# Optimization experiments

Measured on AMD Instinct MI355X. Metric: run time of the kernel, lower is better.

Reference implementation:

```python
import jax, jax.numpy as jnp
import numpy as np

B, T, N, M = 128, 128, 32, 128  # batch, window(input_len), driving_series, hidden_size


def _lstm_cell(x_t, h, c, Wih, Whh, bih, bhh):
    # PyTorch gate order: i, f, g, o
    g = x_t @ Wih.T + bih + h @ Whh.T + bhh
    i, f, gg, o = jnp.split(g, 4, axis=-1)
    c = jax.nn.sigmoid(f) * c + jax.nn.sigmoid(i) * jnp.tanh(gg)
    h = jax.nn.sigmoid(o) * jnp.tanh(c)
    return h, c


def _lstm_seq(x, Wih, Whh, bih, bhh):
    # x: [B,T,n] -> outputs [B,T,m], zero init state
    Bc = x.shape[0]
    m = Whh.shape[1]
    def step(carry, x_t):
        h, c = carry
        h, c = _lstm_cell(x_t, h, c, Wih, Whh, bih, bhh)
        return (h, c), h
    h0 = jnp.zeros((Bc, m), x.dtype)
    (_, _), ys = jax.lax.scan(step, (h0, h0), jnp.swapaxes(x, 0, 1))
    return jnp.swapaxes(ys, 0, 1)


def _forward(x, Wih0, Whh0, bih0, bhh0, We, Ue, Ve,
             Wg, bg, Wa, ba,
             Wih1, Whh1, bih1, bhh1, Wih2, Whh2, bih2, bhh2):
    Bc, Tc, n = x.shape
    m = Whh0.shape[1]
    ux = jnp.einsum('btn,mn->btm', x, Ue)  # Ue(x), constant across steps

    def step(carry, x_t):
        h, c = carry
        hs = jnp.concatenate([h, c], axis=-1)              # [B,2m]
        e = jnp.tanh(ux + (hs @ We.T)[:, None, :]) @ Ve[0]  # [B,T]
        a = jax.nn.softmax(e, axis=1)
        ia_t = jnp.einsum('bt,btn->bn', a, x)              # attended input at step t
        h, c = _lstm_cell(x_t, h, c, Wih0, Whh0, bih0, bhh0)
        return (h, c), ia_t

    h0 = jnp.zeros((Bc, m), x.dtype)
    (_, _), ia = jax.lax.scan(step, (h0, h0), jnp.swapaxes(x, 0, 1))
    input_attention = jnp.swapaxes(ia, 0, 1)               # [B,T,n]

    # self (spatial) attention, fully vectorized over t
    g = jnp.tanh(jnp.einsum('btn,mn->btm', x, Wg) + bg)
    a = jax.nn.sigmoid(jnp.einsum('btm,nm->btn', g, Wa) + ba)
    self_attention = a * x                                  # [B,T,n]

    out1 = _lstm_seq(input_attention, Wih1, Whh1, bih1, bhh1)
    out2 = _lstm_seq(self_attention, Wih2, Whh2, bih2, bhh2)
    return jnp.concatenate([out1, out2], axis=-1)           # [B,T,2m]


def setup_inputs() -> dict:
    key = jax.random.key(0)
    ks = jax.random.split(key, 20)
    stdv = 1.0 / np.sqrt(M)
    u = lambda k, shp: jax.random.uniform(k, shp, jnp.float32, -stdv, stdv)
    inp = {
        'x': jax.random.normal(ks[0], (B, T, N), jnp.float32),
        'Wih0': u(ks[1], (4 * M, N)), 'Whh0': u(ks[2], (4 * M, M)),
        'bih0': u(ks[3], (4 * M,)), 'bhh0': u(ks[4], (4 * M,)),
        'We': u(ks[5], (M, 2 * M)), 'Ue': u(ks[6], (M, N)), 'Ve': u(ks[7], (1, M)),
        'Wg': u(ks[8], (M, N)), 'bg': u(ks[9], (M,)),
        'Wa': u(ks[10], (N, M)), 'ba': u(ks[11], (N,)),
        'Wih1': u(ks[12], (4 * M, N)), 'Whh1': u(ks[13], (4 * M, M)),
        'bih1': u(ks[14], (4 * M,)), 'bhh1': u(ks[15], (4 * M,)),
        'Wih2': u(ks[16], (4 * M, N)), 'Whh2': u(ks[17], (4 * M, M)),
        'bih2': u(ks[18], (4 * M,)), 'bhh2': u(ks[19], (4 * M,)),
    }
    return inp


def reference(x, Wih0, Whh0, bih0, bhh0, We, Ue, Ve, Wg, bg, Wa, ba,
              Wih1, Whh1, bih1, bhh1, Wih2, Whh2, bih2, bhh2):
    return _forward(x, Wih0, Whh0, bih0, bhh0, We, Ue, Ve, Wg, bg, Wa, ba,
                    Wih1, Whh1, bih1, bhh1, Wih2, Whh2, bih2, bhh2)
```

## Files before the change

kernel.cpp:

```cpp
#include <hip/hip_runtime.h>

#define DI __device__ __forceinline__

DI float fsig(float v)  { return 1.0f / (1.0f + __expf(-v)); }
DI float ftanh(float v) { return 1.0f - 2.0f / (__expf(2.0f * v) + 1.0f); }

template <int MODE>
DI void lstm_scan(const float* __restrict__ xin,
                  const float* __restrict__ Wih,
                  const float* __restrict__ Whh,
                  const float* __restrict__ bih,
                  const float* __restrict__ bhh,
                  float* __restrict__ rec,
                  float* __restrict__ outp,
                  float* lds)
{
    const int tid = threadIdx.x;
    float* xl  = lds;
    float* h   = lds + 4096;
    float* c   = lds + 4224;
    float* act = lds + 4352;

    for (int i = tid; i < 4096; i += 512) xl[i] = xin[i];
    if (tid < 128) { h[tid] = 0.f; c[tid] = 0.f; }

    float4 wi[8], wh[32];
    {
        const float4* p = (const float4*)(Wih + tid * 32);
        #pragma unroll
        for (int i = 0; i < 8; ++i) wi[i] = p[i];
        const float4* q2 = (const float4*)(Whh + tid * 128);
        #pragma unroll
        for (int i = 0; i < 32; ++i) wh[i] = q2[i];
    }
    const float bias = bih[tid] + bhh[tid];
    const int gate = tid >> 7;
    __syncthreads();

    for (int t = 0; t < 128; ++t) {
        if (MODE == 0) {
            if (tid < 256) rec[t * 256 + tid] = (tid < 128) ? h[tid] : c[tid - 128];
        }
        float acc = bias;
        const float4* x4 = (const float4*)(xl + t * 32);
        #pragma unroll
        for (int i = 0; i < 8; ++i) {
            float4 v = x4[i];
            acc += wi[i].x * v.x + wi[i].y * v.y + wi[i].z * v.z + wi[i].w * v.w;
        }
        const float4* h4 = (const float4*)h;
        #pragma unroll
        for (int i = 0; i < 32; ++i) {
            float4 v = h4[i];
            acc += wh[i].x * v.x + wh[i].y * v.y + wh[i].z * v.z + wh[i].w * v.w;
        }
        float a = (gate == 2) ? ftanh(acc) : fsig(acc);
        act[tid] = a;
        __syncthreads();
        if (tid < 128) {
            float iv = act[tid], fv = act[128 + tid], gv = act[256 + tid], ov = act[384 + tid];
            float cn = fv * c[tid] + iv * gv;
            float hn = ov * ftanh(cn);
            c[tid] = cn; h[tid] = hn;
            if (MODE == 1) outp[t * 256 + tid] = hn;
        }
        __syncthreads();
    }
}

DI void selfatt_body(const float* __restrict__ x, const float* __restrict__ Wg,
                     const float* __restrict__ bg, const float* __restrict__ Wa,
                     const float* __restrict__ ba, float* __restrict__ sa,
                     int b, float* s)
{
    float* xl  = s;
    float* Wgl = s + 4224;
    float* WaT = s + 8448;
    float* bgl = s + 12672;
    float* bal = s + 12800;
    float* gl  = s + 12832;
    float* pp  = s + 13344;

    const int tid = threadIdx.x;
    for (int i = tid; i < 4096; i += 512) {
        int r = i >> 5, n = i & 31;
        xl[r * 33 + n]  = x[b * 4096 + i];
        Wgl[r * 33 + n] = Wg[i];
        WaT[(i & 127) * 33 + (i >> 7)] = Wa[i];
    }
    if (tid < 128) bgl[tid] = bg[tid];
    else if (tid < 160) bal[tid - 128] = ba[tid - 128];
    __syncthreads();

    const int tl = tid >> 7;
    for (int it = 0; it < 32; ++it) {
        {   const int m = tid & 127;
            const int t = it * 4 + tl;
            float acc = bgl[m];
            #pragma unroll
            for (int n = 0; n < 32; ++n) acc += xl[t * 33 + n] * Wgl[m * 33 + n];
            gl[tl * 128 + m] = ftanh(acc);
        }
        __syncthreads();
        {   const int n = tid & 31, c = (tid >> 5) & 3;
            float acc = 0.f;
            #pragma unroll
            for (int j = 0; j < 32; ++j) {
                int m = c * 32 + j;
                acc += gl[tl * 128 + m] * WaT[m * 33 + n];
            }
            pp[(tl * 4 + c) * 32 + n] = acc;
        }
        __syncthreads();
        if (tid < 128) {
            const int tl2 = tid >> 5, n = tid & 31;
            const int t = it * 4 + tl2;
            float sv = pp[(tl2 * 4 + 0) * 32 + n] + pp[(tl2 * 4 + 1) * 32 + n]
                     + pp[(tl2 * 4 + 2) * 32 + n] + pp[(tl2 * 4 + 3) * 32 + n] + bal[n];
            sa[b * 4096 + t * 32 + n] = fsig(sv) * xl[t * 33 + n];
        }
        __syncthreads();
    }
}

__global__ __launch_bounds__(512)
void kA_lstm0_sa(const float* __restrict__ x,
                 const float* __restrict__ Wih0, const float* __restrict__ Whh0,
                 const float* __restrict__ bih0, const float* __restrict__ bhh0,
                 const float* __restrict__ Wg, const float* __restrict__ bg,
                 const float* __restrict__ Wa, const float* __restrict__ ba,
                 float* __restrict__ rec, float* __restrict__ sa)
{
    __shared__ float smem[13856];
    const int blk = blockIdx.x;
    if (blk < 128) {
        lstm_scan<0>(x + blk * 4096, Wih0, Whh0, bih0, bhh0,
                     rec + blk * 32768, nullptr, smem);
    } else {
        selfatt_body(x, Wg, bg, Wa, ba, sa, blk - 128, smem);
    }
}

__global__ __launch_bounds__(512)
void kC_lstm12(const float* __restrict__ ia, const float* __restrict__ sa,
               const float* __restrict__ Wih1, const float* __restrict__ Whh1,
               const float* __restrict__ bih1, const float* __restrict__ bhh1,
               const float* __restrict__ Wih2, const float* __restrict__ Whh2,
               const float* __restrict__ bih2, const float* __restrict__ bhh2,
               float* __restrict__ out)
{
    __shared__ float smem[4864];
    const int blk = blockIdx.x;
    if (blk < 128) {
        lstm_scan<1>(ia + blk * 4096, Wih1, Whh1, bih1, bhh1,
                     nullptr, out + blk * 32768, smem);
    } else {
        const int b = blk - 128;
        lstm_scan<1>(sa + b * 4096, Wih2, Whh2, bih2, bhh2,
                     nullptr, out + b * 32768 + 128, smem);
    }
}

__global__ __launch_bounds__(512, 4)
void kB_attn(const float* __restrict__ x,
             const float* __restrict__ Ue,
             const float* __restrict__ We,
             const float* __restrict__ Ve,
             const float* __restrict__ rec,
             float* __restrict__ ia)
{
    __shared__ float xl[4608];
    __shared__ float wl[4608];
    __shared__ float ubuf[4608];
    __shared__ float ev[128];
    __shared__ float av[128];
    __shared__ float iap[576];
    __shared__ float wred[2];
    __shared__ float wsum[2];

    const int tid = threadIdx.x;
    const int b  = blockIdx.x >> 2;
    const int tc = blockIdx.x & 3;
    const int ta = tid >> 2;
    const int q  = tid & 3;

    float4 wer[16];
    {
        const float4* p = (const float4*)(We + tid * 64);
        #pragma unroll
        for (int i = 0; i < 16; ++i) wer[i] = p[i];
    }
    for (int i = tid; i < 4096; i += 512)
        xl[(i >> 5) * 36 + (i & 31)] = x[b * 4096 + i];

    const long rbase = (long)b * 32768 + (long)tc * 32 * 256;
    for (int h2 = 0; h2 < 2; ++h2) {
        __syncthreads();
        #pragma unroll
        for (int s = 0; s < 8; ++s) {
            int f = tid + 512 * s;
            int tl = f >> 8, k = f & 255;
            ubuf[tl * 272 + (k >> 6) * 68 + (k & 63)] =
                rec[rbase + (h2 * 16 + tl) * 256 + k];
        }
        __syncthreads();
        for (int tl = 0; tl < 16; ++tl) {
            const float4* hp = (const float4*)(ubuf + tl * 272 + q * 68);
            float acc = 0.f;
            #pragma unroll
            for (int i = 0; i < 16; ++i) {
                float4 v = hp[i];
                acc += wer[i].x * v.x + wer[i].y * v.y + wer[i].z * v.z + wer[i].w * v.w;
            }
            acc += __shfl_xor(acc, 1);
            acc += __shfl_xor(acc, 2);
            if (q == 0)
                wl[(h2 * 16 + tl) * 144 + (ta & 3) * 36 + (ta >> 2)] = 2.0f * acc;
        }
    }
    __syncthreads();

    for (int i = tid; i < 4096; i += 512)
        ubuf[(i >> 5) * 36 + (i & 31)] = Ue[i];
    __syncthreads();

    float uxr[32];
    {
        float xr[32];
        const float4* xp = (const float4*)(xl + ta * 36);
        #pragma unroll
        for (int i = 0; i < 8; ++i) {
            float4 v = xp[i];
            xr[4*i] = v.x; xr[4*i+1] = v.y; xr[4*i+2] = v.z; xr[4*i+3] = v.w;
        }
        #pragma unroll
        for (int j = 0; j < 32; ++j) {
            const float4* up = (const float4*)(ubuf + (4 * j + q) * 36);
            float acc = 0.f;
            #pragma unroll
            for (int i = 0; i < 8; ++i) {
                float4 v = up[i];
                acc += xr[4*i] * v.x + xr[4*i+1] * v.y + xr[4*i+2] * v.z + xr[4*i+3] * v.w;
            }
            uxr[j] = 2.0f * acc;
        }
    }

    float ver[32];
    #pragma unroll
    for (int j = 0; j < 32; ++j) ver[j] = Ve[4 * j + q];
    float VeTot;
    {
        float vs = 0.f;
        #pragma unroll
        for (int j = 0; j < 32; ++j) vs += ver[j];
        vs += __shfl_xor(vs, 1);
        vs += __shfl_xor(vs, 2);
        VeTot = vs;
    }

    for (int tl = 0; tl < 32; ++tl) {
        const int t = tc * 32 + tl;
        float acc2 = 0.f;
        const float4* wr = (const float4*)(wl + tl * 144 + q * 36);
        #pragma unroll
        for (int j4 = 0; j4 < 8; ++j4) {
            float4 w4 = wr[j4];
            {   float zs = uxr[4*j4+0] + w4.x;
                acc2 += ver[4*j4+0] * __fdividef(2.0f, __expf(zs) + 1.0f); }
            {   float zs = uxr[4*j4+1] + w4.y;
                acc2 += ver[4*j4+1] * __fdividef(2.0f, __expf(zs) + 1.0f); }
            {   float zs = uxr[4*j4+2] + w4.z;
                acc2 += ver[4*j4+2] * __fdividef(2.0f, __expf(zs) + 1.0f); }
            {   float zs = uxr[4*j4+3] + w4.w;
                acc2 += ver[4*j4+3] * __fdividef(2.0f, __expf(zs) + 1.0f); }
        }
        acc2 += __shfl_xor(acc2, 1);
        acc2 += __shfl_xor(acc2, 2);
        if (q == 0) ev[ta] = VeTot - acc2;
        __syncthreads();

        float vv = 0.f, aa;
        if (tid < 128) {
            vv = ev[tid];
            float m2 = vv;
            #pragma unroll
            for (int o = 32; o > 0; o >>= 1) m2 = fmaxf(m2, __shfl_xor(m2, o));
            if ((tid & 63) == 0) wred[tid >> 6] = m2;
        }
        __syncthreads();
        if (tid < 128) {
            float M = fmaxf(wred[0], wred[1]);
            aa = __expf(vv - M);
            av[tid] = aa;
            float s = aa;
            #pragma unroll
            for (int o = 32; o > 0; o >>= 1) s += __shfl_xor(s, o);
            if ((tid & 63) == 0) wsum[tid >> 6] = s;
        }
        __syncthreads();
        {   const int n = tid & 31, g = tid >> 5;
            float accp = 0.f;
            #pragma unroll
            for (int jj = 0; jj < 8; ++jj) {
                const int t2 = g * 8 + jj;
                accp += av[t2] * xl[t2 * 36 + n];
            }
            iap[g * 36 + n] = accp;
        }
        __syncthreads();
        if (tid < 32) {
            float s = 0.f;
            #pragma unroll
            for (int g = 0; g < 16; ++g) s += iap[g * 36 + tid];
            float scale = __fdividef(1.0f, wsum[0] + wsum[1]);
            ia[((long)b * 128 + t) * 32 + tid] = s * scale;
        }
    }
}

extern "C" void kernel_launch(void* const* d_in, const int* in_sizes, int n_in,
                              void* d_out, int out_size, void* d_ws, size_t ws_size,
                              hipStream_t stream)
{
    const float* x    = (const float*)d_in[0];
    const float* Wih0 = (const float*)d_in[1];
    const float* Whh0 = (const float*)d_in[2];
    const float* bih0 = (const float*)d_in[3];
    const float* bhh0 = (const float*)d_in[4];
    const float* We   = (const float*)d_in[5];
    const float* Ue   = (const float*)d_in[6];
    const float* Ve   = (const float*)d_in[7];
    const float* Wg   = (const float*)d_in[8];
    const float* bg   = (const float*)d_in[9];
    const float* Wa   = (const float*)d_in[10];
    const float* ba   = (const float*)d_in[11];
    const float* Wih1 = (const float*)d_in[12];
    const float* Whh1 = (const float*)d_in[13];
    const float* bih1 = (const float*)d_in[14];
    const float* bhh1 = (const float*)d_in[15];
    const float* Wih2 = (const float*)d_in[16];
    const float* Whh2 = (const float*)d_in[17];
    const float* bih2 = (const float*)d_in[18];
    const float* bhh2 = (const float*)d_in[19];

    float* out = (float*)d_out;
    float* ws  = (float*)d_ws;
    float* sa  = ws;
    float* rec = ws + 524288;
    float* iaw = ws + 4718592;

    kA_lstm0_sa<<<256, 512, 0, stream>>>(x, Wih0, Whh0, bih0, bhh0,
                                         Wg, bg, Wa, ba, rec, sa);
    kB_attn<<<512, 512, 0, stream>>>(x, Ue, We, Ve, rec, iaw);
    kC_lstm12<<<256, 512, 0, stream>>>(iaw, sa, Wih1, Whh1, bih1, bhh1,
                                       Wih2, Whh2, bih2, bhh2, out);
}
```

Baseline: 528.9 us.

## Split LSTM dot products 8-way over 1024 threads and restructure attention kernel

Each LSTM scan now uses 1024 threads. The 160-element input and hidden dot product is split into eight 20-element partial sums that are reduced through LDS, and gate combination uses shuffles with c kept in registers. The We projection of [h,c] moves into a new precomputation kernel that overwrites rec in place. The attention kernel is reorganised to tile Ue·x and the tanh scores across threads, so the softmax is computed for 32 timesteps at once instead of once per step. Divisions become hardware reciprocals. The intent is a shorter serial critical path per LSTM step and fewer per-step barriers in attention, at the cost of an extra kernel launch, an extra round trip through rec, and one block per CU.

Measured after the change: 682.4 us. 29.0% more time.

```diff
diff --git a/kernel.cpp b/kernel.cpp
--- a/kernel.cpp
+++ b/kernel.cpp
@@ -2,67 +2,101 @@
 
 #define DI __device__ __forceinline__
 
-DI float fsig(float v)  { return 1.0f / (1.0f + __expf(-v)); }
-DI float ftanh(float v) { return 1.0f - 2.0f / (__expf(2.0f * v) + 1.0f); }
+DI float frcp(float v)  { return __builtin_amdgcn_rcpf(v); }
+DI float fsig(float v)  { return frcp(1.0f + __expf(-v)); }
+DI float ftanh(float v) { return 1.0f - 2.0f * frcp(__expf(2.0f * v) + 1.0f); }
+
+DI float dot4(float4 a, float4 b) { return a.x*b.x + a.y*b.y + a.z*b.z + a.w*b.w; }
 
 template <int MODE>
-DI void lstm_scan(const float* __restrict__ xin,
-                  const float* __restrict__ Wih,
-                  const float* __restrict__ Whh,
-                  const float* __restrict__ bih,
-                  const float* __restrict__ bhh,
-                  float* __restrict__ rec,
-                  float* __restrict__ outp,
-                  float* lds)
+DI void lstm_scan8(const float* __restrict__ xin,
+                   const float* __restrict__ Wih,
+                   const float* __restrict__ Whh,
+                   const float* __restrict__ bih,
+                   const float* __restrict__ bhh,
+                   float* __restrict__ rec,
+                   float* __restrict__ outp,
+                   float* lds)
 {
     const int tid = threadIdx.x;
-    float* xl  = lds;
-    float* h   = lds + 4096;
-    float* c   = lds + 4224;
-    float* act = lds + 4352;
-
-    for (int i = tid; i < 4096; i += 512) xl[i] = xin[i];
-    if (tid < 128) { h[tid] = 0.f; c[tid] = 0.f; }
-
-    float4 wi[8], wh[32];
-    {
-        const float4* p = (const float4*)(Wih + tid * 32);
-        #pragma unroll
-        for (int i = 0; i < 8; ++i) wi[i] = p[i];
-        const float4* q2 = (const float4*)(Whh + tid * 128);
-        #pragma unroll
-        for (int i = 0; i < 32; ++i) wh[i] = q2[i];
-    }
-    const float bias = bih[tid] + bhh[tid];
-    const int gate = tid >> 7;
+    const int r0 = tid & 127;
+    const int kq = tid >> 7;
+    float* xl = lds;
+    float* hl = lds + 4096;
+    float* pl = lds + 4224;
+
+    for (int i = tid; i < 4096; i += 1024) xl[i] = xin[i];
+    if (tid < 128) hl[tid] = 0.f;
+
+    float4 w[4][5];
+    #pragma unroll
+    for (int g = 0; g < 4; ++g) {
+        const int r = g * 128 + r0;
+        if (kq == 0) {
+            const float4* p = (const float4*)(Wih + r * 32);
+            #pragma unroll
+            for (int j = 0; j < 5; ++j) w[g][j] = p[j];
+        } else if (kq == 1) {
+            const float4* p = (const float4*)(Wih + r * 32 + 20);
+            w[g][0] = p[0]; w[g][1] = p[1]; w[g][2] = p[2];
+            const float4* p2 = (const float4*)(Whh + r * 128);
+            w[g][3] = p2[0]; w[g][4] = p2[1];
+        } else {
+            const float4* p = (const float4*)(Whh + r * 128 + 20 * kq - 32);
+            #pragma unroll
+            for (int j = 0; j < 5; ++j) w[g][j] = p[j];
+        }
+    }
+
+    const int rr = (tid & 511) >> 2;
+    const int gg = tid & 3;
+    float bias = 0.f, creg = 0.f, hreg = 0.f;
+    if (tid < 512) bias = bih[gg * 128 + rr] + bhh[gg * 128 + rr];
+    const float nl_a = (gg == 2) ? 2.0f : 1.0f;
+    const float nl_b = (gg == 2) ? -1.0f : 0.0f;
     __syncthreads();
 
     for (int t = 0; t < 128; ++t) {
-        if (MODE == 0) {
-            if (tid < 256) rec[t * 256 + tid] = (tid < 128) ? h[tid] : c[tid - 128];
-        }
-        float acc = bias;
-        const float4* x4 = (const float4*)(xl + t * 32);
-        #pragma unroll
-        for (int i = 0; i < 8; ++i) {
-            float4 v = x4[i];
-            acc += wi[i].x * v.x + wi[i].y * v.y + wi[i].z * v.z + wi[i].w * v.w;
-        }
-        const float4* h4 = (const float4*)h;
-        #pragma unroll
-        for (int i = 0; i < 32; ++i) {
-            float4 v = h4[i];
-            acc += wh[i].x * v.x + wh[i].y * v.y + wh[i].z * v.z + wh[i].w * v.w;
-        }
-        float a = (gate == 2) ? ftanh(acc) : fsig(acc);
-        act[tid] = a;
-        __syncthreads();
-        if (tid < 128) {
-            float iv = act[tid], fv = act[128 + tid], gv = act[256 + tid], ov = act[384 + tid];
-            float cn = fv * c[tid] + iv * gv;
-            float hn = ov * ftanh(cn);
-            c[tid] = cn; h[tid] = hn;
-            if (MODE == 1) outp[t * 256 + tid] = hn;
+        float4 z0, z1, z2, z3, z4;
+        if (kq == 0) {
+            const float4* x4 = (const float4*)(xl + t * 32);
+            z0 = x4[0]; z1 = x4[1]; z2 = x4[2]; z3 = x4[3]; z4 = x4[4];
+        } else if (kq == 1) {
+            const float4* x4 = (const float4*)(xl + t * 32 + 20);
+            z0 = x4[0]; z1 = x4[1]; z2 = x4[2];
+            const float4* h4 = (const float4*)hl;
+            z3 = h4[0]; z4 = h4[1];
+        } else {
+            const float4* h4 = (const float4*)(hl + 20 * kq - 32);
+            z0 = h4[0]; z1 = h4[1]; z2 = h4[2]; z3 = h4[3]; z4 = h4[4];
+        }
+        #pragma unroll
+        for (int g = 0; g < 4; ++g) {
+            float a = dot4(w[g][0], z0) + dot4(w[g][1], z1) + dot4(w[g][2], z2)
+                    + dot4(w[g][3], z3) + dot4(w[g][4], z4);
+            pl[kq * 576 + g * 144 + r0] = a;
+        }
+        __syncthreads();
+        if (tid < 512) {
+            float s = bias;
+            #pragma unroll
+            for (int k = 0; k < 8; ++k) s += pl[k * 576 + gg * 144 + rr];
+            float sg = frcp(1.0f + __expf(-(nl_a * s)));
+            float val = nl_a * sg + nl_b;
+            float v1 = __shfl_xor(val, 1);
+            float v2 = __shfl_xor(val, 2);
+            float v3 = __shfl_xor(val, 3);
+            if (gg == 0) {
+                if (MODE == 0) {
+                    rec[t * 256 + rr]       = hreg;
+                    rec[t * 256 + 128 + rr] = creg;
+                }
+                float cn = v1 * creg + val * v2;
+                float hn = v3 * ftanh(cn);
+                creg = cn; hreg = hn;
+                hl[rr] = hn;
+                if (MODE == 1) outp[t * 256 + rr] = hn;
+            }
         }
         __syncthreads();
     }
@@ -79,10 +113,10 @@
     float* bgl = s + 12672;
     float* bal = s + 12800;
     float* gl  = s + 12832;
-    float* pp  = s + 13344;
+    float* pp  = s + 13856;
 
     const int tid = threadIdx.x;
-    for (int i = tid; i < 4096; i += 512) {
+    for (int i = tid; i < 4096; i += 1024) {
         int r = i >> 5, n = i & 31;
         xl[r * 33 + n]  = x[b * 4096 + i];
         Wgl[r * 33 + n] = Wg[i];
@@ -93,9 +127,9 @@
     __syncthreads();
 
     const int tl = tid >> 7;
-    for (int it = 0; it < 32; ++it) {
+    for (int it = 0; it < 16; ++it) {
         {   const int m = tid & 127;
-            const int t = it * 4 + tl;
+            const int t = it * 8 + tl;
             float acc = bgl[m];
             #pragma unroll
             for (int n = 0; n < 32; ++n) acc += xl[t * 33 + n] * Wgl[m * 33 + n];
@@ -112,9 +146,9 @@
             pp[(tl * 4 + c) * 32 + n] = acc;
         }
         __syncthreads();
-        if (tid < 128) {
+        if (tid < 256) {
             const int tl2 = tid >> 5, n = tid & 31;
-            const int t = it * 4 + tl2;
+            const int t = it * 8 + tl2;
             float sv = pp[(tl2 * 4 + 0) * 32 + n] + pp[(tl2 * 4 + 1) * 32 + n]
                      + pp[(tl2 * 4 + 2) * 32 + n] + pp[(tl2 * 4 + 3) * 32 + n] + bal[n];
             sa[b * 4096 + t * 32 + n] = fsig(sv) * xl[t * 33 + n];
@@ -123,199 +157,204 @@
     }
 }
 
-__global__ __launch_bounds__(512)
-void kA_lstm0_sa(const float* __restrict__ x,
+__global__ __launch_bounds__(1024, 1)
+void k1_lstm0_sa(const float* __restrict__ x,
                  const float* __restrict__ Wih0, const float* __restrict__ Whh0,
                  const float* __restrict__ bih0, const float* __restrict__ bhh0,
                  const float* __restrict__ Wg, const float* __restrict__ bg,
                  const float* __restrict__ Wa, const float* __restrict__ ba,
                  float* __restrict__ rec, float* __restrict__ sa)
 {
-    __shared__ float smem[13856];
+    __shared__ float smem[14880];
     const int blk = blockIdx.x;
     if (blk < 128) {
-        lstm_scan<0>(x + blk * 4096, Wih0, Whh0, bih0, bhh0,
-                     rec + blk * 32768, nullptr, smem);
+        lstm_scan8<0>(x + blk * 4096, Wih0, Whh0, bih0, bhh0,
+                      rec + blk * 32768, nullptr, smem);
     } else {
         selfatt_body(x, Wg, bg, Wa, ba, sa, blk - 128, smem);
     }
 }
 
-__global__ __launch_bounds__(512)
-void kC_lstm12(const float* __restrict__ ia, const float* __restrict__ sa,
+__global__ __launch_bounds__(1024, 1)
+void k3_lstm12(const float* __restrict__ ia, const float* __restrict__ sa,
                const float* __restrict__ Wih1, const float* __restrict__ Whh1,
                const float* __restrict__ bih1, const float* __restrict__ bhh1,
                const float* __restrict__ Wih2, const float* __restrict__ Whh2,
                const float* __restrict__ bih2, const float* __restrict__ bhh2,
                float* __restrict__ out)
 {
-    __shared__ float smem[4864];
+    __shared__ float smem[8832];
     const int blk = blockIdx.x;
     if (blk < 128) {
-        lstm_scan<1>(ia + blk * 4096, Wih1, Whh1, bih1, bhh1,
-                     nullptr, out + blk * 32768, smem);
+        lstm_scan8<1>(ia + blk * 4096, Wih1, Whh1, bih1, bhh1,
+                      nullptr, out + blk * 32768, smem);
     } else {
         const int b = blk - 128;
-        lstm_scan<1>(sa + b * 4096, Wih2, Whh2, bih2, bhh2,
-                     nullptr, out + b * 32768 + 128, smem);
-    }
-}
-
-__global__ __launch_bounds__(512, 4)
+        lstm_scan8<1>(sa + b * 4096, Wih2, Whh2, bih2, bhh2,
+                      nullptr, out + b * 32768 + 128, smem);
+    }
+}
+
+__global__ __launch_bounds__(512, 1)
+void kP_w2(const float* __restrict__ We,
+           float* __restrict__ rec)
+{
+    __shared__ float smem[12544];
+    float* hsB  = smem;
+    float* wbuf = smem + 8320;
+    const int tid = threadIdx.x;
+    const int b = blockIdx.x;
+    const int m = tid >> 2, q = tid & 3;
+
+    float4 wer[16];
+    {
+        const float4* p = (const float4*)(We + m * 256 + q * 64);
+        #pragma unroll
+        for (int i = 0; i < 16; ++i) wer[i] = p[i];
+    }
+    #pragma unroll
+    for (int i = 0; i < 16; i += 4) {
+        asm volatile("" : "+v"(wer[i].x), "+v"(wer[i].y), "+v"(wer[i].z), "+v"(wer[i].w),
+                          "+v"(wer[i+1].x), "+v"(wer[i+1].y), "+v"(wer[i+1].z), "+v"(wer[i+1].w),
+                          "+v"(wer[i+2].x), "+v"(wer[i+2].y), "+v"(wer[i+2].z), "+v"(wer[i+2].w),
+                          "+v"(wer[i+3].x), "+v"(wer[i+3].y), "+v"(wer[i+3].z), "+v"(wer[i+3].w));
+    }
+
+    for (int tb = 0; tb < 4; ++tb) {
+        __syncthreads();
+        for (int i = tid; i < 8192; i += 512)
+            hsB[(i >> 8) * 260 + (i & 255)] = rec[(long)b * 32768 + (tb * 32 + (i >> 8)) * 256 + (i & 255)];
+        __syncthreads();
+        for (int tl = 0; tl < 32; ++tl) {
+            const float4* h4 = (const float4*)(hsB + tl * 260 + q * 64);
+            float acc = 0.f;
+            #pragma unroll
+            for (int i = 0; i < 16; ++i) acc += dot4(wer[i], h4[i]);
+            acc += __shfl_xor(acc, 1);
+            acc += __shfl_xor(acc, 2);
+            if (q == 0) wbuf[tl * 132 + m] = acc;
+        }
+        __syncthreads();
+        for (int i = tid; i < 4096; i += 512)
+            rec[(long)b * 32768 + tb * 4096 + i] = 2.0f * wbuf[(i >> 7) * 132 + (i & 127)];
+    }
+}
+
+__global__ __launch_bounds__(512, 2)
 void kB_attn(const float* __restrict__ x,
              const float* __restrict__ Ue,
-             const float* __restrict__ We,
              const float* __restrict__ Ve,
-             const float* __restrict__ rec,
+             const float* __restrict__ w2g,
              float* __restrict__ ia)
 {
     __shared__ float xl[4608];
-    __shared__ float wl[4608];
-    __shared__ float ubuf[4608];
-    __shared__ float ev[128];
-    __shared__ float av[128];
+    __shared__ float wl[4224];
+    __shared__ float uxc[4224];
+    __shared__ float UeAv[4608];
+    __shared__ float vel[128];
+    __shared__ float sinv[32];
     __shared__ float iap[576];
-    __shared__ float wred[2];
-    __shared__ float wsum[2];
 
     const int tid = threadIdx.x;
     const int b  = blockIdx.x >> 2;
     const int tc = blockIdx.x & 3;
-    const int ta = tid >> 2;
-    const int q  = tid & 3;
-
-    float4 wer[16];
+
+    for (int i = tid; i < 4096; i += 512) {
+        xl[(i >> 5) * 36 + (i & 31)]   = x[b * 4096 + i];
+        UeAv[(i >> 5) * 36 + (i & 31)] = Ue[i];
+        wl[(i >> 7) * 132 + (i & 127)] = w2g[(long)b * 32768 + (tc * 32 + (i >> 7)) * 128 + (i & 127)];
+    }
+    if (tid < 128) vel[tid] = 2.0f * Ve[tid];
+    __syncthreads();
+
+    const int ts = tid & 127, mg = tid >> 7;
+    float4 xr[8];
     {
-        const float4* p = (const float4*)(We + tid * 64);
-        #pragma unroll
-        for (int i = 0; i < 16; ++i) wer[i] = p[i];
-    }
-    for (int i = tid; i < 4096; i += 512)
-        xl[(i >> 5) * 36 + (i & 31)] = x[b * 4096 + i];
-
-    const long rbase = (long)b * 32768 + (long)tc * 32 * 256;
-    for (int h2 = 0; h2 < 2; ++h2) {
-        __syncthreads();
-        #pragma unroll
-        for (int s = 0; s < 8; ++s) {
-            int f = tid + 512 * s;
-            int tl = f >> 8, k = f & 255;
-            ubuf[tl * 272 + (k >> 6) * 68 + (k & 63)] =
-                rec[rbase + (h2 * 16 + tl) * 256 + k];
-        }
-        __syncthreads();
-        for (int tl = 0; tl < 16; ++tl) {
-            const float4* hp = (const float4*)(ubuf + tl * 272 + q * 68);
+        const float4* xp = (const float4*)(xl + ts * 36);
+        #pragma unroll
+        for (int i = 0; i < 8; ++i) xr[i] = xp[i];
+    }
+    float VeTot = 0.f;
+    for (int i = 0; i < 128; ++i) VeTot += vel[i];
+    VeTot *= 0.5f;
+
+    const int tp = tid >> 5, tg = tid & 31;
+    const int t0 = 2 * tp, t1 = t0 + 1;
+    float s0[4] = {0.f, 0.f, 0.f, 0.f};
+    float s1[4] = {0.f, 0.f, 0.f, 0.f};
+
+    for (int mc = 0; mc < 4; ++mc) {
+        #pragma unroll
+        for (int j = 0; j < 8; ++j) {
+            const int ml = mg * 8 + j;
+            const float4* u4 = (const float4*)(UeAv + (mc * 32 + ml) * 36);
             float acc = 0.f;
             #pragma unroll
-            for (int i = 0; i < 16; ++i) {
-                float4 v = hp[i];
-                acc += wer[i].x * v.x + wer[i].y * v.y + wer[i].z * v.z + wer[i].w * v.w;
-            }
-            acc += __shfl_xor(acc, 1);
-            acc += __shfl_xor(acc, 2);
-            if (q == 0)
-                wl[(h2 * 16 + tl) * 144 + (ta & 3) * 36 + (ta >> 2)] = 2.0f * acc;
-        }
-    }
+            for (int i = 0; i < 8; ++i) acc += dot4(xr[i], u4[i]);
+            uxc[ml * 132 + ts] = 2.0f * acc;
+        }
+        __syncthreads();
+        #pragma unroll 8
+        for (int ml = 0; ml < 32; ++ml) {
+            const int m = mc * 32 + ml;
+            const float vm = vel[m];
+            const float w0 = wl[t0 * 132 + m];
+            const float w1 = wl[t1 * 132 + m];
+            const float4 u4 = *(const float4*)(uxc + ml * 132 + 4 * tg);
+            s0[0] += vm * frcp(__expf(u4.x + w0) + 1.0f);
+            s0[1] += vm * frcp(__expf(u4.y + w0) + 1.0f);
+            s0[2] += vm * frcp(__expf(u4.z + w0) + 1.0f);
+            s0[3] += vm * frcp(__expf(u4.w + w0) + 1.0f);
+            s1[0] += vm * frcp(__expf(u4.x + w1) + 1.0f);
+            s1[1] += vm * frcp(__expf(u4.y + w1) + 1.0f);
+            s1[2] += vm * frcp(__expf(u4.z + w1) + 1.0f);
+            s1[3] += vm * frcp(__expf(u4.w + w1) + 1.0f);
+        }
+        __syncthreads();
+    }
+
+    float e0[4], e1[4];
+    #pragma unroll
+    for (int j = 0; j < 4; ++j) { e0[j] = VeTot - s0[j]; e1[j] = VeTot - s1[j]; }
+    float M0 = fmaxf(fmaxf(e0[0], e0[1]), fmaxf(e0[2], e0[3]));
+    float M1 = fmaxf(fmaxf(e1[0], e1[1]), fmaxf(e1[2], e1[3]));
+    #pragma unroll
+    for (int o = 1; o < 32; o <<= 1) {
+        M0 = fmaxf(M0, __shfl_xor(M0, o));
+        M1 = fmaxf(M1, __shfl_xor(M1, o));
+    }
+    float a00 = __expf(e0[0] - M0), a01 = __expf(e0[1] - M0);
+    float a02 = __expf(e0[2] - M0), a03 = __expf(e0[3] - M0);
+    float a10 = __expf(e1[0] - M1), a11 = __expf(e1[1] - M1);
+    float a12 = __expf(e1[2] - M1), a13 = __expf(e1[3] - M1);
+    float S0 = a00 + a01 + a02 + a03;
+    float S1 = a10 + a11 + a12 + a13;
+    #pragma unroll
+    for (int o = 1; o < 32; o <<= 1) {
+        S0 += __shfl_xor(S0, o);
+        S1 += __shfl_xor(S1, o);
+    }
+    float* av = UeAv;
+    *(float4*)(av + t0 * 128 + 4 * tg) = make_float4(a00, a01, a02, a03);
+    *(float4*)(av + t1 * 128 + 4 * tg) = make_float4(a10, a11, a12, a13);
+    if (tg == 0) { sinv[t0] = frcp(S0); sinv[t1] = frcp(S1); }
     __syncthreads();
 
-    for (int i = tid; i < 4096; i += 512)
-        ubuf[(i >> 5) * 36 + (i & 31)] = Ue[i];
-    __syncthreads();
-
-    float uxr[32];
-    {
-        float xr[32];
-        const float4* xp = (const float4*)(xl + ta * 36);
-        #pragma unroll
-        for (int i = 0; i < 8; ++i) {
-            float4 v = xp[i];
-            xr[4*i] = v.x; xr[4*i+1] = v.y; xr[4*i+2] = v.z; xr[4*i+3] = v.w;
-        }
-        #pragma unroll
-        for (int j = 0; j < 32; ++j) {
-            const float4* up = (const float4*)(ubuf + (4 * j + q) * 36);
-            float acc = 0.f;
-            #pragma unroll
-            for (int i = 0; i < 8; ++i) {
-                float4 v = up[i];
-                acc += xr[4*i] * v.x + xr[4*i+1] * v.y + xr[4*i+2] * v.z + xr[4*i+3] * v.w;
-            }
-            uxr[j] = 2.0f * acc;
-        }
-    }
-
-    float ver[32];
-    #pragma unroll
-    for (int j = 0; j < 32; ++j) ver[j] = Ve[4 * j + q];
-    float VeTot;
-    {
-        float vs = 0.f;
-        #pragma unroll
-        for (int j = 0; j < 32; ++j) vs += ver[j];
-        vs += __shfl_xor(vs, 1);
-        vs += __shfl_xor(vs, 2);
-        VeTot = vs;
-    }
-
+    const int gph = tid >> 5, n = tid & 31;
     for (int tl = 0; tl < 32; ++tl) {
-        const int t = tc * 32 + tl;
-        float acc2 = 0.f;
-        const float4* wr = (const float4*)(wl + tl * 144 + q * 36);
-        #pragma unroll
-        for (int j4 = 0; j4 < 8; ++j4) {
-            float4 w4 = wr[j4];
-            {   float zs = uxr[4*j4+0] + w4.x;
-                acc2 += ver[4*j4+0] * __fdividef(2.0f, __expf(zs) + 1.0f); }
-            {   float zs = uxr[4*j4+1] + w4.y;
-                acc2 += ver[4*j4+1] * __fdividef(2.0f, __expf(zs) + 1.0f); }
-            {   float zs = uxr[4*j4+2] + w4.z;
-                acc2 += ver[4*j4+2] * __fdividef(2.0f, __expf(zs) + 1.0f); }
-            {   float zs = uxr[4*j4+3] + w4.w;
-                acc2 += ver[4*j4+3] * __fdividef(2.0f, __expf(zs) + 1.0f); }
-        }
-        acc2 += __shfl_xor(acc2, 1);
-        acc2 += __shfl_xor(acc2, 2);
-        if (q == 0) ev[ta] = VeTot - acc2;
-        __syncthreads();
-
-        float vv = 0.f, aa;
-        if (tid < 128) {
-            vv = ev[tid];
-            float m2 = vv;
-            #pragma unroll
-            for (int o = 32; o > 0; o >>= 1) m2 = fmaxf(m2, __shfl_xor(m2, o));
-            if ((tid & 63) == 0) wred[tid >> 6] = m2;
-        }
-        __syncthreads();
-        if (tid < 128) {
-            float M = fmaxf(wred[0], wred[1]);
-            aa = __expf(vv - M);
-            av[tid] = aa;
-            float s = aa;
-            #pragma unroll
-            for (int o = 32; o > 0; o >>= 1) s += __shfl_xor(s, o);
-            if ((tid & 63) == 0) wsum[tid >> 6] = s;
-        }
-        __syncthreads();
-        {   const int n = tid & 31, g = tid >> 5;
-            float accp = 0.f;
-            #pragma unroll
-            for (int jj = 0; jj < 8; ++jj) {
-                const int t2 = g * 8 + jj;
-                accp += av[t2] * xl[t2 * 36 + n];
-            }
-            iap[g * 36 + n] = accp;
-        }
+        float acc = 0.f;
+        #pragma unroll
+        for (int j = 0; j < 8; ++j)
+            acc += av[tl * 128 + gph * 8 + j] * xl[(gph * 8 + j) * 36 + n];
+        iap[gph * 36 + n] = acc;
         __syncthreads();
         if (tid < 32) {
             float s = 0.f;
             #pragma unroll
             for (int g = 0; g < 16; ++g) s += iap[g * 36 + tid];
-            float scale = __fdividef(1.0f, wsum[0] + wsum[1]);
-            ia[((long)b * 128 + t) * 32 + tid] = s * scale;
-        }
+            ia[((long)(b * 128 + tc * 32 + tl)) * 32 + tid] = s * sinv[tl];
+        }
+        __syncthreads();
     }
 }
 
@@ -350,9 +389,10 @@
     float* rec = ws + 524288;
     float* iaw = ws + 4718592;
 
-    kA_lstm0_sa<<<256, 512, 0, stream>>>(x, Wih0, Whh0, bih0, bhh0,
-                                         Wg, bg, Wa, ba, rec, sa);
-    kB_attn<<<512, 512, 0, stream>>>(x, Ue, We, Ve, rec, iaw);
-    kC_lstm12<<<256, 512, 0, stream>>>(iaw, sa, Wih1, Whh1, bih1, bhh1,
-                                       Wih2, Whh2, bih2, bhh2, out);
-}
+    k1_lstm0_sa<<<256, 1024, 0, stream>>>(x, Wih0, Whh0, bih0, bhh0,
+                                          Wg, bg, Wa, ba, rec, sa);
+    kP_w2<<<128, 512, 0, stream>>>(We, rec);
+    kB_attn<<<512, 512, 0, stream>>>(x, Ue, Ve, rec, iaw);
+    k3_lstm12<<<256, 1024, 0, stream>>>(iaw, sa, Wih1, Whh1, bih1, bhh1,
+                                        Wih2, Whh2, bih2, bhh2, out);
+}
```
